# Kernel tuning notes

Hardware: AMD Instinct MI355X
Metric: run time of the kernel (lower is better)

Reference implementation:

```python
import jax, jax.numpy as jnp
import numpy as np

ATTN_MASK_VALUE = -1e10
N, D_IN, D_HEAD, D_OUT = 8192, 1024, 128, 1024


def setup_inputs() -> dict:
    key = jax.random.key(0)
    k_x, k_wqkv, k_bqkv, k_wo, k_bo = jax.random.split(key, 5)
    x = jax.random.normal(k_x, (N, D_IN), dtype=jnp.float32)
    # flax Dense default: lecun_normal kernel, zeros bias; use scaled normal for test
    w_qkv = jax.random.normal(k_wqkv, (D_IN, 3 * D_HEAD), dtype=jnp.float32) / np.sqrt(D_IN)
    b_qkv = jnp.zeros((3 * D_HEAD,), dtype=jnp.float32)
    w_out = jax.random.normal(k_wo, (D_HEAD, D_OUT), dtype=jnp.float32) / np.sqrt(D_HEAD)
    b_out = jnp.zeros((D_OUT,), dtype=jnp.float32)
    return {"x": x, "w_qkv": w_qkv, "b_qkv": b_qkv, "w_out": w_out, "b_out": b_out}


def reference(x, w_qkv, b_qkv, w_out, b_out):
    n = x.shape[0]
    scale = D_HEAD ** (-0.5)
    qkv = x @ w_qkv + b_qkv                      # [n, 3*dh]
    q, k, v = jnp.split(qkv, 3, axis=-1)         # each [n, dh]
    sim = jnp.einsum('id,jd->ij', q, k) * scale  # [n, n]
    mask = jnp.triu(jnp.ones((n, n), dtype=bool), 1)
    sim = jnp.where(mask, ATTN_MASK_VALUE, sim)
    attn = jax.nn.softmax(sim, axis=-1)
    out = jnp.einsum('ij,jd->id', attn, v)       # [n, dh]
    return out @ w_out + b_out                   # [n, d_out]
```

## Files before the change

kernel.cpp:

```cpp
#include <hip/hip_runtime.h>
#include <stdint.h>

typedef __attribute__((ext_vector_type(4))) float f32x4;
typedef __attribute__((ext_vector_type(8))) __bf16 bf16x8;

#define MFMA16(a, b, c) __builtin_amdgcn_mfma_f32_16x16x32_bf16(a, b, c, 0, 0, 0)
#define GLOAD16(g, l)                                                              \
  __builtin_amdgcn_global_load_lds(                                                \
      (const __attribute__((address_space(1))) unsigned int*)(g),                  \
      (__attribute__((address_space(3))) unsigned int*)(l), 16, 0, 0)
#define EXP2F(x) __builtin_amdgcn_exp2f(x)

static __device__ __forceinline__ unsigned short f2b(float f) {
  unsigned int u = __float_as_uint(f);
  u += 0x7fff + ((u >> 16) & 1);
  return (unsigned short)(u >> 16);
}

#define NROWS 8192
#define DIN   1024
#define DH    128
#define DOUT  1024

__global__ void k_convert_w(const float* __restrict__ wqkv, const float* __restrict__ wout,
                            unsigned short* __restrict__ wqkvT, unsigned short* __restrict__ woutT) {
  int idx = blockIdx.x * 256 + threadIdx.x;
  if (idx < 384 * 1024) {
    int n = idx >> 10, k = idx & 1023;
    wqkvT[idx] = f2b(wqkv[k * 384 + n]);
  }
  int idx2 = idx - 384 * 1024;
  if (idx2 >= 0 && idx2 < 1024 * 128) {
    int n = idx2 >> 7, k = idx2 & 127;
    woutT[idx2] = f2b(wout[k * 1024 + n]);
  }
}

__global__ void k_convert_x(const float* __restrict__ x, unsigned short* __restrict__ xb) {
  int i = (blockIdx.x * 256 + threadIdx.x) * 4;
  float4 v = *reinterpret_cast<const float4*>(x + i);
  ushort4 h;
  h.x = f2b(v.x); h.y = f2b(v.y); h.z = f2b(v.z); h.w = f2b(v.w);
  *reinterpret_cast<ushort4*>(xb + i) = h;
}

__launch_bounds__(256, 2)
__global__ void k_qkv_gemm(const unsigned short* __restrict__ xb, const unsigned short* __restrict__ wT,
                           const float* __restrict__ bqkv,
                           unsigned short* __restrict__ Qb, unsigned short* __restrict__ Kb,
                           unsigned short* __restrict__ Vb) {
  const int hb = blockIdx.x;
  const int xcd = hb & 7, jj = hb >> 3;
  const int tau = xcd * 24 + jj;
  const int bn = tau % 3, bm = tau / 3;
  const int tid = threadIdx.x;
  const int lane = tid & 63, w = tid >> 6;
  const int l15 = lane & 15, g = lane >> 4;
  const int wm = (w >> 1) * 64, wn = (w & 1) * 64;
  const int row0 = bm * 128, col0 = bn * 128;

  __shared__ __align__(16) char Ash[2][16384];
  __shared__ __align__(16) char Bsh[2][16384];

  f32x4 acc[4][4] = {};

#define QKV_STAGE(k0, buf)                                                          \
  {                                                                                 \
    _Pragma("unroll")                                                               \
    for (int j2 = 0; j2 < 4; ++j2) {                                                \
      int idx = j2 * 256 + tid;                                                     \
      int r = idx >> 3, gg = idx & 7, sgg = gg ^ (r & 7);                           \
      GLOAD16(xb + (size_t)(row0 + r) * DIN + (k0) + sgg * 8, Ash[buf] + idx * 16); \
      GLOAD16(wT + (size_t)(col0 + r) * DIN + (k0) + sgg * 8, Bsh[buf] + idx * 16); \
    }                                                                               \
  }

  QKV_STAGE(0, 0);
  __syncthreads();
  int cur = 0;
  for (int k0 = 0; k0 < DIN; k0 += 64) {
    if (k0 + 64 < DIN) QKV_STAGE(k0 + 64, cur ^ 1);
#pragma unroll
    for (int ksl = 0; ksl < 2; ++ksl) {
      bf16x8 af[4], bfr[4];
#pragma unroll
      for (int i = 0; i < 4; ++i) {
        int r = wm + i * 16 + l15;
        int ba = r * 128 + ksl * 64 + g * 16;
        af[i] = *reinterpret_cast<bf16x8*>(Ash[cur] + (ba ^ ((r & 7) << 4)));
        int n = wn + i * 16 + l15;
        int bb = n * 128 + ksl * 64 + g * 16;
        bfr[i] = *reinterpret_cast<bf16x8*>(Bsh[cur] + (bb ^ ((n & 7) << 4)));
      }
#pragma unroll
      for (int i = 0; i < 4; ++i)
#pragma unroll
        for (int jn = 0; jn < 4; ++jn)
          acc[i][jn] = MFMA16(af[i], bfr[jn], acc[i][jn]);
    }
    __syncthreads();
    cur ^= 1;
  }

  unsigned short* outb = (bn == 0) ? Qb : (bn == 1 ? Kb : Vb);
#pragma unroll
  for (int i = 0; i < 4; ++i)
#pragma unroll
    for (int jn = 0; jn < 4; ++jn)
#pragma unroll
      for (int r = 0; r < 4; ++r) {
        int grow = row0 + wm + i * 16 + g * 4 + r;
        int lcol = wn + jn * 16 + l15;
        float vv = acc[i][jn][r] + bqkv[bn * 128 + lcol];
        outb[(size_t)grow * DH + lcol] = f2b(vv);
      }
}

__global__ void k_transpose_v(const unsigned short* __restrict__ V, unsigned short* __restrict__ VT) {
  __shared__ __align__(16) unsigned short t[64 * 128];
  const int b = blockIdx.x;
  const int tid = threadIdx.x;
  const int kv0 = b * 64;
#pragma unroll
  for (int j = 0; j < 4; ++j) {
    int c = j * 256 + tid;
    int r = c >> 4, cc = (c & 15) * 8;
    uint4 v = *reinterpret_cast<const uint4*>(V + (size_t)(kv0 + r) * DH + cc);
    int col = (cc + ((r >> 3) & 7) * 8) & 127;
    *reinterpret_cast<uint4*>(&t[r * 128 + col]) = v;
  }
  __syncthreads();
#pragma unroll
  for (int j = 0; j < 4; ++j) {
    int c = j * 256 + tid;
    int d = c >> 3, kk = (c & 7) * 8;
    unsigned short tmp[8];
#pragma unroll
    for (int e = 0; e < 8; ++e) {
      int r = kk + e;
      int col = (d + ((r >> 3) & 7) * 8) & 127;
      tmp[e] = t[r * 128 + col];
    }
    *reinterpret_cast<uint4*>(VT + (size_t)d * NROWS + kv0 + kk) = *reinterpret_cast<uint4*>(tmp);
  }
}

__launch_bounds__(256, 2)
__global__ void k_flash(const unsigned short* __restrict__ Q, const unsigned short* __restrict__ Kg,
                        const unsigned short* __restrict__ VT,
                        float* __restrict__ Opart, float* __restrict__ MLpart, int LJ) {
  const int ci = blockIdx.x;
  const int t = (int)(gridDim.y - 1) - (int)blockIdx.y;
  const int J = 1 << LJ;
  if (ci * J > t) return;
  const int qb = t * 64;
  const int ks = ci * (J << 6);
  const int ke = min(ks + (J << 6), qb + 64);
  const int nsteps = (ke - ks) >> 6;

  const int a = t >> LJ, b = t & (J - 1);
  const int slot = t + ((J * a * (a - 1)) >> 1) + a * b + ci;

  const int tid = threadIdx.x;
  const int lane = tid & 63, w = tid >> 6;
  const int l15 = lane & 15, g = lane >> 4;

  __shared__ __align__(16) char Ksh[2][16384];
  __shared__ __align__(16) char Vsh[2][16384];
  __shared__ __align__(16) char Psh[4][2048];

  const int qrow = qb + w * 16 + l15;
  bf16x8 qf[4];
#pragma unroll
  for (int d = 0; d < 4; ++d)
    qf[d] = *reinterpret_cast<const bf16x8*>(Q + (size_t)qrow * DH + d * 32 + g * 8);

  f32x4 acco[8] = {};
  float m = -1e30f, l = 0.f;
  const float c2 = 0.08838834764831843f * 1.4426950408889634f;
  const int wmax = qb + w * 16 + 15;

#define FL_STAGE(kv0, buf)                                                            \
  {                                                                                   \
    _Pragma("unroll")                                                                 \
    for (int j2 = 0; j2 < 4; ++j2) {                                                  \
      int idx = j2 * 256 + tid;                                                       \
      int r = idx >> 4, gg = idx & 15, sgg = gg ^ (r & 7);                            \
      GLOAD16(Kg + (size_t)((kv0) + r) * DH + sgg * 8, Ksh[buf] + idx * 16);          \
    }                                                                                 \
    _Pragma("unroll")                                                                 \
    for (int j2 = 0; j2 < 4; ++j2) {                                                  \
      int idx = j2 * 256 + tid;                                                       \
      int d = idx >> 3, gg = idx & 7, sgg = gg ^ (d & 7);                             \
      GLOAD16(VT + (size_t)d * NROWS + (kv0) + sgg * 8, Vsh[buf] + idx * 16);         \
    }                                                                                 \
  }

  FL_STAGE(ks, 0);
  __syncthreads();
  int cur = 0;

  for (int s = 0; s < nsteps; ++s) {
    const int kv0 = ks + (s << 6);
    if (s + 1 < nsteps) FL_STAGE(kv0 + 64, cur ^ 1);

    if (kv0 <= wmax) {
      f32x4 accs[4] = {};
#pragma unroll
      for (int jc = 0; jc < 4; ++jc) {
#pragma unroll
        for (int d = 0; d < 4; ++d) {
          int r = jc * 16 + l15;
          int byte = r * 256 + d * 64 + g * 16; byte ^= (r & 7) << 4;
          bf16x8 kf = *reinterpret_cast<bf16x8*>(Ksh[cur] + byte);
          accs[jc] = MFMA16(kf, qf[d], accs[jc]);
        }
      }

      float p[4][4];
      float mx = -3e38f;
#pragma unroll
      for (int jc = 0; jc < 4; ++jc)
#pragma unroll
        for (int r = 0; r < 4; ++r) {
          float sv = accs[jc][r] * c2;
          int kk = kv0 + jc * 16 + (g << 2) + r;
          sv = (kk <= qrow) ? sv : -3e38f;
          p[jc][r] = sv;
          mx = fmaxf(mx, sv);
        }
      mx = fmaxf(mx, __shfl_xor(mx, 16));
      mx = fmaxf(mx, __shfl_xor(mx, 32));
      float mnew = fmaxf(m, mx);
      float fac = EXP2F(m - mnew);
      float ps = 0.f;
#pragma unroll
      for (int jc = 0; jc < 4; ++jc)
#pragma unroll
        for (int r = 0; r < 4; ++r) {
          float e = EXP2F(p[jc][r] - mnew);
          p[jc][r] = e;
          ps += e;
        }
      ps += __shfl_xor(ps, 16);
      ps += __shfl_xor(ps, 32);
      l = l * fac + ps;
      m = mnew;
#pragma unroll
      for (int dc = 0; dc < 8; ++dc)
#pragma unroll
        for (int r = 0; r < 4; ++r) acco[dc][r] *= fac;

      char* Pw = Psh[w];
#pragma unroll
      for (int jc = 0; jc < 4; ++jc) {
        ushort4 pb;
        pb.x = f2b(p[jc][0]); pb.y = f2b(p[jc][1]);
        pb.z = f2b(p[jc][2]); pb.w = f2b(p[jc][3]);
        int byte = l15 * 128 + jc * 32 + g * 8; byte ^= (l15 & 7) << 4;
        *reinterpret_cast<ushort4*>(Pw + byte) = pb;
      }
      __asm__ volatile("s_waitcnt lgkmcnt(0)" ::: "memory");
      __builtin_amdgcn_sched_barrier(0);

      bf16x8 pf[2];
#pragma unroll
      for (int ks2 = 0; ks2 < 2; ++ks2) {
        int byte = l15 * 128 + ks2 * 64 + g * 16; byte ^= (l15 & 7) << 4;
        pf[ks2] = *reinterpret_cast<bf16x8*>(Pw + byte);
      }
#pragma unroll
      for (int dc = 0; dc < 8; ++dc) {
#pragma unroll
        for (int ks2 = 0; ks2 < 2; ++ks2) {
          int vr = dc * 16 + l15;
          int byte = vr * 128 + ks2 * 64 + g * 16; byte ^= (vr & 7) << 4;
          bf16x8 vf = *reinterpret_cast<bf16x8*>(Vsh[cur] + byte);
          acco[dc] = MFMA16(vf, pf[ks2], acco[dc]);
        }
      }
    }
    __syncthreads();
    cur ^= 1;
  }

  const size_t orow = (size_t)slot * 64 + w * 16 + l15;
#pragma unroll
  for (int dc = 0; dc < 8; ++dc) {
    f32x4 o4;
#pragma unroll
    for (int r = 0; r < 4; ++r) o4[r] = acco[dc][r];
    *reinterpret_cast<f32x4*>(Opart + orow * DH + dc * 16 + (g << 2)) = o4;
  }
  if (g == 0) {
    MLpart[orow * 2 + 0] = m;
    MLpart[orow * 2 + 1] = l;
  }
}

__global__ void k_merge(const float* __restrict__ Opart, const float* __restrict__ MLpart,
                        unsigned short* __restrict__ O, int LJ) {
  int tg = blockIdx.x * 256 + threadIdx.x;
  int row = tg >> 5, d4 = (tg & 31) * 4;
  int t = row >> 6;
  int J = 1 << LJ;
  int a = t >> LJ, b = t & (J - 1);
  int base = t + ((J * a * (a - 1)) >> 1) + a * b;
  int nc = a + 1;
  int rowin = row & 63;
  float M = -3e38f;
  for (int i = 0; i < nc; ++i) M = fmaxf(M, MLpart[((size_t)(base + i) * 64 + rowin) * 2]);
  float L = 0.f;
  f32x4 acc = {};
  for (int i = 0; i < nc; ++i) {
    size_t sr = (size_t)(base + i) * 64 + rowin;
    float mi = MLpart[sr * 2];
    float li = MLpart[sr * 2 + 1];
    float wg = EXP2F(mi - M);
    L += li * wg;
    f32x4 o = *reinterpret_cast<const f32x4*>(Opart + sr * DH + d4);
#pragma unroll
    for (int e = 0; e < 4; ++e) acc[e] += wg * o[e];
  }
  float inv = 1.f / L;
  ushort4 hv;
  hv.x = f2b(acc[0] * inv); hv.y = f2b(acc[1] * inv);
  hv.z = f2b(acc[2] * inv); hv.w = f2b(acc[3] * inv);
  *reinterpret_cast<ushort4*>(O + (size_t)row * DH + d4) = hv;
}

__launch_bounds__(256, 2)
__global__ void k_out_gemm(const unsigned short* __restrict__ O, const unsigned short* __restrict__ wT,
                           const float* __restrict__ bout, float* __restrict__ out) {
  const int hb = blockIdx.x;
  const int xcd = hb & 7, jj = hb >> 3;
  const int tau = xcd * 256 + jj;
  const int bn = tau & 15, bm = tau >> 4;
  const int tid = threadIdx.x;
  const int lane = tid & 63, w = tid >> 6;
  const int l15 = lane & 15, g = lane >> 4;
  const int wm = (w >> 1) * 32, wn = (w & 1) * 32;
  const int row0 = bm * 64, col0 = bn * 64;

  __shared__ __align__(16) char Ash[16384];
  __shared__ __align__(16) char Bsh[16384];

#pragma unroll
  for (int j = 0; j < 4; ++j) {
    int idx = j * 256 + tid;
    int r = idx >> 4, gg = idx & 15;
    int sgg = gg ^ (r & 7);
    GLOAD16(O + (size_t)(row0 + r) * DH + sgg * 8, Ash + idx * 16);
    GLOAD16(wT + (size_t)(col0 + r) * DH + sgg * 8, Bsh + idx * 16);
  }
  __syncthreads();

  f32x4 acc[2][2] = {};
#pragma unroll
  for (int ksl = 0; ksl < 4; ++ksl) {
    bf16x8 af[2], bfr[2];
#pragma unroll
    for (int i = 0; i < 2; ++i) {
      int r = wm + i * 16 + l15;
      int ba = r * 256 + ksl * 64 + g * 16;
      af[i] = *reinterpret_cast<bf16x8*>(Ash + (ba ^ ((r & 7) << 4)));
      int n = wn + i * 16 + l15;
      int bb = n * 256 + ksl * 64 + g * 16;
      bfr[i] = *reinterpret_cast<bf16x8*>(Bsh + (bb ^ ((n & 7) << 4)));
    }
#pragma unroll
    for (int i = 0; i < 2; ++i)
#pragma unroll
      for (int jn = 0; jn < 2; ++jn)
        acc[i][jn] = MFMA16(af[i], bfr[jn], acc[i][jn]);
  }

#pragma unroll
  for (int i = 0; i < 2; ++i)
#pragma unroll
    for (int jn = 0; jn < 2; ++jn)
#pragma unroll
      for (int r = 0; r < 4; ++r) {
        int grow = row0 + wm + i * 16 + g * 4 + r;
        int gcol = col0 + wn + jn * 16 + l15;
        out[(size_t)grow * DOUT + gcol] = acc[i][jn][r] + bout[gcol];
      }
}

extern "C" void kernel_launch(void* const* d_in, const int* in_sizes, int n_in,
                              void* d_out, int out_size, void* d_ws, size_t ws_size,
                              hipStream_t stream) {
  const float* x    = (const float*)d_in[0];
  const float* wqkv = (const float*)d_in[1];
  const float* bqkv = (const float*)d_in[2];
  const float* wout = (const float*)d_in[3];
  const float* bout = (const float*)d_in[4];
  float* out = (float*)d_out;

  size_t fixed = 786432 + 262144 + (size_t)NROWS * DIN * 2 + (size_t)5 * NROWS * DH * 2;
  int LJ = 3;
  size_t slots = 0;
  for (; LJ <= 7; ++LJ) {
    int J = 1 << LJ, A = 128 >> LJ;
    slots = 128 + (size_t)J * A * (A - 1) / 2;
    size_t need = fixed + slots * ((size_t)64 * DH * 4 + 64 * 8);
    if (need <= ws_size || LJ == 7) break;
  }

  char* ws = (char*)d_ws;
  size_t off = 0;
  unsigned short* wqkvT = (unsigned short*)(ws + off); off += (size_t)384 * 1024 * 2;
  unsigned short* woutT = (unsigned short*)(ws + off); off += (size_t)1024 * 128 * 2;
  unsigned short* xb  = (unsigned short*)(ws + off); off += (size_t)NROWS * DIN * 2;
  unsigned short* Qb  = (unsigned short*)(ws + off); off += (size_t)NROWS * DH * 2;
  unsigned short* Kb  = (unsigned short*)(ws + off); off += (size_t)NROWS * DH * 2;
  unsigned short* Vb  = (unsigned short*)(ws + off); off += (size_t)NROWS * DH * 2;
  unsigned short* VTb = (unsigned short*)(ws + off); off += (size_t)NROWS * DH * 2;
  unsigned short* Ob  = (unsigned short*)(ws + off); off += (size_t)NROWS * DH * 2;
  float* Opart  = (float*)(ws + off); off += slots * (size_t)64 * DH * 4;
  float* MLpart = (float*)(ws + off); off += slots * (size_t)64 * 8;

  k_convert_w<<<2048, 256, 0, stream>>>(wqkv, wout, wqkvT, woutT);
  k_convert_x<<<(NROWS * DIN) / 1024, 256, 0, stream>>>(x, xb);
  k_qkv_gemm<<<192, 256, 0, stream>>>(xb, wqkvT, bqkv, Qb, Kb, Vb);
  k_transpose_v<<<128, 256, 0, stream>>>(Vb, VTb);
  k_flash<<<dim3(128 >> LJ, 128), 256, 0, stream>>>(Qb, Kb, VTb, Opart, MLpart, LJ);
  k_merge<<<(NROWS * 32) / 256, 256, 0, stream>>>(Opart, MLpart, Ob, LJ);
  k_out_gemm<<<2048, 256, 0, stream>>>(Ob, woutT, bout, out);
}
```

Measured before the change: 126.4 us.

## Software-pipeline PV with next QK, read V from global, tile weight conversion

The flash kernel stops staging V through LDS. Each step issues the previous block's P·V MFMAs, with V fragments loaded straight from global/L2, between the current QK^T and its softmax, and a final PV runs after the loop. This frees LDS and raises the launch-bounds occupancy target to 4 blocks per CU. The per-wave causal skip (kv0 <= wmax) is removed, and the weight-convert kernel becomes a 64x64 LDS-tiled transpose with coalesced float4 loads, launched on 128 blocks. The risks are higher global/L2 traffic for V, extra register pressure, and the removed wave-level skip adding wasted work on diagonal blocks.

```diff
diff --git a/kernel.cpp b/kernel.cpp
--- a/kernel.cpp
+++ b/kernel.cpp
@@ -24,15 +24,37 @@
 
 __global__ void k_convert_w(const float* __restrict__ wqkv, const float* __restrict__ wout,
                             unsigned short* __restrict__ wqkvT, unsigned short* __restrict__ woutT) {
-  int idx = blockIdx.x * 256 + threadIdx.x;
-  if (idx < 384 * 1024) {
-    int n = idx >> 10, k = idx & 1023;
-    wqkvT[idx] = f2b(wqkv[k * 384 + n]);
-  }
-  int idx2 = idx - 384 * 1024;
-  if (idx2 >= 0 && idx2 < 1024 * 128) {
-    int n = idx2 >> 7, k = idx2 & 127;
-    woutT[idx2] = f2b(wout[k * 1024 + n]);
+  __shared__ float t[64][65];
+  const int bid = blockIdx.x;
+  const float* src;
+  unsigned short* dst;
+  int k0, n0, sstride, dstride;
+  if (bid < 96) {
+    int kt = bid / 6, nt = bid % 6;
+    k0 = kt * 64; n0 = nt * 64;
+    src = wqkv; sstride = 384; dst = wqkvT; dstride = 1024;
+  } else {
+    int b2 = bid - 96;
+    int kt = b2 & 1, nt = b2 >> 1;
+    k0 = kt * 64; n0 = nt * 64;
+    src = wout; sstride = 1024; dst = woutT; dstride = 128;
+  }
+  const int tid = threadIdx.x;
+  const int r = tid >> 4, c4 = (tid & 15) * 4;
+#pragma unroll
+  for (int j = 0; j < 4; ++j) {
+    int rr = r + j * 16;
+    float4 v = *reinterpret_cast<const float4*>(src + (size_t)(k0 + rr) * sstride + n0 + c4);
+    t[rr][c4 + 0] = v.x; t[rr][c4 + 1] = v.y; t[rr][c4 + 2] = v.z; t[rr][c4 + 3] = v.w;
+  }
+  __syncthreads();
+#pragma unroll
+  for (int j = 0; j < 4; ++j) {
+    int rn = r + j * 16;
+    ushort4 h;
+    h.x = f2b(t[c4 + 0][rn]); h.y = f2b(t[c4 + 1][rn]);
+    h.z = f2b(t[c4 + 2][rn]); h.w = f2b(t[c4 + 3][rn]);
+    *reinterpret_cast<ushort4*>(dst + (size_t)(n0 + rn) * dstride + k0 + c4) = h;
   }
 }
 
@@ -145,7 +167,7 @@
   }
 }
 
-__launch_bounds__(256, 2)
+__launch_bounds__(256, 4)
 __global__ void k_flash(const unsigned short* __restrict__ Q, const unsigned short* __restrict__ Kg,
                         const unsigned short* __restrict__ VT,
                         float* __restrict__ Opart, float* __restrict__ MLpart, int LJ) {
@@ -166,7 +188,6 @@
   const int l15 = lane & 15, g = lane >> 4;
 
   __shared__ __align__(16) char Ksh[2][16384];
-  __shared__ __align__(16) char Vsh[2][16384];
   __shared__ __align__(16) char Psh[4][2048];
 
   const int qrow = qb + w * 16 + l15;
@@ -178,9 +199,8 @@
   f32x4 acco[8] = {};
   float m = -1e30f, l = 0.f;
   const float c2 = 0.08838834764831843f * 1.4426950408889634f;
-  const int wmax = qb + w * 16 + 15;
-
-#define FL_STAGE(kv0, buf)                                                            \
+
+#define FL_STAGE_K(kv0, buf)                                                          \
   {                                                                                   \
     _Pragma("unroll")                                                                 \
     for (int j2 = 0; j2 < 4; ++j2) {                                                  \
@@ -188,101 +208,98 @@
       int r = idx >> 4, gg = idx & 15, sgg = gg ^ (r & 7);                            \
       GLOAD16(Kg + (size_t)((kv0) + r) * DH + sgg * 8, Ksh[buf] + idx * 16);          \
     }                                                                                 \
+  }
+
+  const unsigned short* vbase = VT + (size_t)l15 * NROWS + g * 8;
+  char* Pw = Psh[w];
+
+#define PV_STEP(kvp)                                                                  \
+  {                                                                                   \
+    bf16x8 pf0, pf1;                                                                  \
+    { int byte = l15 * 128 + g * 16; byte ^= (l15 & 7) << 4;                          \
+      pf0 = *reinterpret_cast<bf16x8*>(Pw + byte); }                                  \
+    { int byte = l15 * 128 + 64 + g * 16; byte ^= (l15 & 7) << 4;                     \
+      pf1 = *reinterpret_cast<bf16x8*>(Pw + byte); }                                  \
     _Pragma("unroll")                                                                 \
-    for (int j2 = 0; j2 < 4; ++j2) {                                                  \
-      int idx = j2 * 256 + tid;                                                       \
-      int d = idx >> 3, gg = idx & 7, sgg = gg ^ (d & 7);                             \
-      GLOAD16(VT + (size_t)d * NROWS + (kv0) + sgg * 8, Vsh[buf] + idx * 16);         \
+    for (int dc = 0; dc < 8; ++dc) {                                                  \
+      const unsigned short* vr = vbase + (size_t)dc * 16 * NROWS + (kvp);             \
+      bf16x8 vf0 = *reinterpret_cast<const bf16x8*>(vr);                              \
+      bf16x8 vf1 = *reinterpret_cast<const bf16x8*>(vr + 32);                         \
+      acco[dc] = MFMA16(vf0, pf0, acco[dc]);                                          \
+      acco[dc] = MFMA16(vf1, pf1, acco[dc]);                                          \
     }                                                                                 \
   }
 
-  FL_STAGE(ks, 0);
+  FL_STAGE_K(ks, 0);
   __syncthreads();
   int cur = 0;
 
   for (int s = 0; s < nsteps; ++s) {
     const int kv0 = ks + (s << 6);
-    if (s + 1 < nsteps) FL_STAGE(kv0 + 64, cur ^ 1);
-
-    if (kv0 <= wmax) {
-      f32x4 accs[4] = {};
-#pragma unroll
-      for (int jc = 0; jc < 4; ++jc) {
-#pragma unroll
-        for (int d = 0; d < 4; ++d) {
-          int r = jc * 16 + l15;
-          int byte = r * 256 + d * 64 + g * 16; byte ^= (r & 7) << 4;
-          bf16x8 kf = *reinterpret_cast<bf16x8*>(Ksh[cur] + byte);
-          accs[jc] = MFMA16(kf, qf[d], accs[jc]);
-        }
-      }
-
-      float p[4][4];
-      float mx = -3e38f;
-#pragma unroll
-      for (int jc = 0; jc < 4; ++jc)
-#pragma unroll
-        for (int r = 0; r < 4; ++r) {
-          float sv = accs[jc][r] * c2;
-          int kk = kv0 + jc * 16 + (g << 2) + r;
-          sv = (kk <= qrow) ? sv : -3e38f;
-          p[jc][r] = sv;
-          mx = fmaxf(mx, sv);
-        }
-      mx = fmaxf(mx, __shfl_xor(mx, 16));
-      mx = fmaxf(mx, __shfl_xor(mx, 32));
-      float mnew = fmaxf(m, mx);
-      float fac = EXP2F(m - mnew);
-      float ps = 0.f;
-#pragma unroll
-      for (int jc = 0; jc < 4; ++jc)
-#pragma unroll
-        for (int r = 0; r < 4; ++r) {
-          float e = EXP2F(p[jc][r] - mnew);
-          p[jc][r] = e;
-          ps += e;
-        }
-      ps += __shfl_xor(ps, 16);
-      ps += __shfl_xor(ps, 32);
-      l = l * fac + ps;
-      m = mnew;
-#pragma unroll
-      for (int dc = 0; dc < 8; ++dc)
-#pragma unroll
-        for (int r = 0; r < 4; ++r) acco[dc][r] *= fac;
-
-      char* Pw = Psh[w];
-#pragma unroll
-      for (int jc = 0; jc < 4; ++jc) {
-        ushort4 pb;
-        pb.x = f2b(p[jc][0]); pb.y = f2b(p[jc][1]);
-        pb.z = f2b(p[jc][2]); pb.w = f2b(p[jc][3]);
-        int byte = l15 * 128 + jc * 32 + g * 8; byte ^= (l15 & 7) << 4;
-        *reinterpret_cast<ushort4*>(Pw + byte) = pb;
-      }
-      __asm__ volatile("s_waitcnt lgkmcnt(0)" ::: "memory");
-      __builtin_amdgcn_sched_barrier(0);
-
-      bf16x8 pf[2];
-#pragma unroll
-      for (int ks2 = 0; ks2 < 2; ++ks2) {
-        int byte = l15 * 128 + ks2 * 64 + g * 16; byte ^= (l15 & 7) << 4;
-        pf[ks2] = *reinterpret_cast<bf16x8*>(Pw + byte);
-      }
-#pragma unroll
-      for (int dc = 0; dc < 8; ++dc) {
-#pragma unroll
-        for (int ks2 = 0; ks2 < 2; ++ks2) {
-          int vr = dc * 16 + l15;
-          int byte = vr * 128 + ks2 * 64 + g * 16; byte ^= (vr & 7) << 4;
-          bf16x8 vf = *reinterpret_cast<bf16x8*>(Vsh[cur] + byte);
-          acco[dc] = MFMA16(vf, pf[ks2], acco[dc]);
-        }
-      }
+    if (s + 1 < nsteps) FL_STAGE_K(kv0 + 64, cur ^ 1);
+
+    f32x4 accs[4] = {};
+#pragma unroll
+    for (int jc = 0; jc < 4; ++jc) {
+#pragma unroll
+      for (int d = 0; d < 4; ++d) {
+        int r = jc * 16 + l15;
+        int byte = r * 256 + d * 64 + g * 16; byte ^= (r & 7) << 4;
+        bf16x8 kf = *reinterpret_cast<bf16x8*>(Ksh[cur] + byte);
+        accs[jc] = MFMA16(kf, qf[d], accs[jc]);
+      }
+    }
+
+    float p[4][4];
+    float mx = -3e38f;
+#pragma unroll
+    for (int jc = 0; jc < 4; ++jc)
+#pragma unroll
+      for (int r = 0; r < 4; ++r) {
+        float sv = accs[jc][r] * c2;
+        int kk = kv0 + jc * 16 + (g << 2) + r;
+        sv = (kk <= qrow) ? sv : -3e38f;
+        p[jc][r] = sv;
+        mx = fmaxf(mx, sv);
+      }
+
+    if (s > 0) PV_STEP(kv0 - 64);
+
+    mx = fmaxf(mx, __shfl_xor(mx, 16));
+    mx = fmaxf(mx, __shfl_xor(mx, 32));
+    float mnew = fmaxf(m, mx);
+    float fac = EXP2F(m - mnew);
+    float ps = 0.f;
+#pragma unroll
+    for (int jc = 0; jc < 4; ++jc)
+#pragma unroll
+      for (int r = 0; r < 4; ++r) {
+        float e = EXP2F(p[jc][r] - mnew);
+        p[jc][r] = e;
+        ps += e;
+      }
+    ps += __shfl_xor(ps, 16);
+    ps += __shfl_xor(ps, 32);
+    l = l * fac + ps;
+    m = mnew;
+#pragma unroll
+    for (int dc = 0; dc < 8; ++dc)
+#pragma unroll
+      for (int r = 0; r < 4; ++r) acco[dc][r] *= fac;
+
+#pragma unroll
+    for (int jc = 0; jc < 4; ++jc) {
+      ushort4 pb;
+      pb.x = f2b(p[jc][0]); pb.y = f2b(p[jc][1]);
+      pb.z = f2b(p[jc][2]); pb.w = f2b(p[jc][3]);
+      int byte = l15 * 128 + jc * 32 + g * 8; byte ^= (l15 & 7) << 4;
+      *reinterpret_cast<ushort4*>(Pw + byte) = pb;
     }
     __syncthreads();
     cur ^= 1;
   }
+
+  PV_STEP(ks + ((nsteps - 1) << 6));
 
   const size_t orow = (size_t)slot * 64 + w * 16 + l15;
 #pragma unroll
@@ -420,7 +437,7 @@
   float* Opart  = (float*)(ws + off); off += slots * (size_t)64 * DH * 4;
   float* MLpart = (float*)(ws + off); off += slots * (size_t)64 * 8;
 
-  k_convert_w<<<2048, 256, 0, stream>>>(wqkv, wout, wqkvT, woutT);
+  k_convert_w<<<128, 256, 0, stream>>>(wqkv, wout, wqkvT, woutT);
   k_convert_x<<<(NROWS * DIN) / 1024, 256, 0, stream>>>(x, xb);
   k_qkv_gemm<<<192, 256, 0, stream>>>(xb, wqkvT, bqkv, Qb, Kb, Vb);
   k_transpose_v<<<128, 256, 0, stream>>>(Vb, VTb);
```

Result: slower. 188.2 us (+48.9%).
